# Kernel optimization log

Measured on AMD Instinct MI355X. Metric: run time of the kernel, lower is better.

## Reference

```python
import jax, jax.numpy as jnp
import numpy as np

N_NODES = 100000
N_EDGES = 1600000
N_GRAPHS = 2048
DIM_IN, DIM_H, DIM_FC, DIM_OUT = 128, 128, 256, 8


def _glorot(key, shape):
    fan_in, fan_out = shape[0], shape[1]
    lim = float(np.sqrt(6.0 / (fan_in + fan_out)))
    return jax.random.uniform(key, shape, jnp.float32, -lim, lim)


def setup_inputs() -> dict:
    key = jax.random.key(0)
    ks = jax.random.split(key, 16)
    x = jax.random.normal(ks[0], (N_NODES, DIM_IN), jnp.float32)
    edge_index = jax.random.randint(ks[1], (2, N_EDGES), 0, N_NODES, jnp.int64)
    batch = jnp.sort(jax.random.randint(ks[2], (N_NODES,), 0, N_GRAPHS, jnp.int64))
    inp = {"x": x, "edge_index": edge_index, "batch": batch}
    # GraphConv layers: W_rel [in,out], W_root [in,out], b [out]
    dims = [(DIM_IN, DIM_H), (DIM_H, DIM_H), (DIM_H, DIM_H), (DIM_H, DIM_H)]
    for i, (di, do) in enumerate(dims, start=1):
        inp[f"W{i}_rel"] = _glorot(ks[2 + 3 * i], (di, do))
        inp[f"W{i}_root"] = _glorot(ks[3 + 3 * i], (di, do))
        inp[f"b{i}"] = jnp.zeros((do,), jnp.float32)
    inp["fc_w"] = _glorot(ks[3], (DIM_H, DIM_FC))
    inp["fc_b"] = jnp.zeros((DIM_FC,), jnp.float32)
    inp["reg_w"] = _glorot(ks[4], (DIM_FC, DIM_OUT))
    inp["reg_b"] = jnp.zeros((DIM_OUT,), jnp.float32)
    return inp


def _graph_conv(x, src, dst, w_rel, w_root, b):
    # PyG GraphConv (aggr='add'): out_i = W_rel @ sum_{j->i} x_j + W_root @ x_i + b
    agg = jax.ops.segment_sum(x[src], dst, num_segments=N_NODES)  # [N, d_in]
    return agg @ w_rel + x @ w_root + b


def reference(x, edge_index, batch,
              W1_rel, W1_root, b1, W2_rel, W2_root, b2,
              W3_rel, W3_root, b3, W4_rel, W4_root, b4,
              fc_w, fc_b, reg_w, reg_b):
    src, dst = edge_index[0], edge_index[1]
    h = jax.nn.relu(_graph_conv(x, src, dst, W1_rel, W1_root, b1))
    h = jax.nn.relu(_graph_conv(h, src, dst, W2_rel, W2_root, b2))
    h = jax.nn.relu(_graph_conv(h, src, dst, W3_rel, W3_root, b3))
    h = jax.nn.relu(_graph_conv(h, src, dst, W4_rel, W4_root, b4))
    # global_mean_pool over graphs
    sums = jax.ops.segment_sum(h, batch, num_segments=N_GRAPHS)  # [G, d]
    cnt = jax.ops.segment_sum(jnp.ones((h.shape[0],), h.dtype), batch,
                              num_segments=N_GRAPHS)
    pooled = sums / jnp.maximum(cnt, 1.0)[:, None]
    # dropout is identity at inference
    hfc = pooled @ fc_w + fc_b
    return hfc @ reg_w + reg_b  # [G, dim_out]
```

## Files before the change

kernel.cpp:

```cpp
#include <hip/hip_runtime.h>

#define N_NODES 100000
#define N_EDGES 1600000
#define N_GRAPHS 2048
#define DIM 128

#define NBUK 196
#define BUKSH 9
#define NCH 256
#define EPB 6250
#define NMAT (NBUK * NCH)

typedef short short8v __attribute__((ext_vector_type(8)));
typedef float float4v __attribute__((ext_vector_type(4)));

__device__ __forceinline__ unsigned short f2bf(float f) {
  union { float f; unsigned u; } x; x.f = f;
  unsigned r = x.u + 0x7fffu + ((x.u >> 16) & 1u);
  return (unsigned short)(r >> 16);
}
__device__ __forceinline__ float bfhi2f(unsigned bits) {
  union { unsigned u; float f; } x; x.u = bits; return x.f;
}
__device__ __forceinline__ void accum8(float* p, uint4 v) {
  p[0] += bfhi2f(v.x << 16); p[1] += bfhi2f(v.x & 0xffff0000u);
  p[2] += bfhi2f(v.y << 16); p[3] += bfhi2f(v.y & 0xffff0000u);
  p[4] += bfhi2f(v.z << 16); p[5] += bfhi2f(v.z & 0xffff0000u);
  p[6] += bfhi2f(v.w << 16); p[7] += bfhi2f(v.w & 0xffff0000u);
}

__global__ __launch_bounds__(256) void k_bcount(const int* __restrict__ dst, int* __restrict__ cntmat) {
  __shared__ int cnt[NBUK];
  int b = blockIdx.x, t = threadIdx.x;
  if (t < NBUK) cnt[t] = 0;
  __syncthreads();
  int e0 = b * EPB;
  for (int j = t; j < EPB; j += 256) atomicAdd(&cnt[dst[e0 + j] >> BUKSH], 1);
  __syncthreads();
  if (t < NBUK) cntmat[t * NCH + b] = cnt[t];
}

__global__ __launch_bounds__(256) void k_scan1g(const int* __restrict__ in, int n,
                                                int* __restrict__ tmp, int* __restrict__ bsum) {
  __shared__ int sh[256];
  int b = blockIdx.x, t = threadIdx.x;
  int base = b * 1024 + t * 4;
  int v[4], s = 0;
#pragma unroll
  for (int i = 0; i < 4; i++) { v[i] = (base + i < n) ? in[base + i] : 0; s += v[i]; }
  sh[t] = s;
  __syncthreads();
  for (int off = 1; off < 256; off <<= 1) {
    int x = (t >= off) ? sh[t - off] : 0;
    __syncthreads();
    sh[t] += x;
    __syncthreads();
  }
  int run = sh[t] - s;
#pragma unroll
  for (int i = 0; i < 4; i++) { run += v[i]; if (base + i < n) tmp[base + i] = run; }
  if (t == 255) bsum[b] = sh[255];
}

__global__ void k_scan2g(int* __restrict__ bsum, int nb) {
  __shared__ int sh[128];
  int t = threadIdx.x;
  int v = (t < nb) ? bsum[t] : 0;
  sh[t] = v;
  __syncthreads();
  for (int off = 1; off < 128; off <<= 1) {
    int x = (t >= off) ? sh[t - off] : 0;
    __syncthreads();
    sh[t] += x;
    __syncthreads();
  }
  if (t < nb) bsum[t] = sh[t] - v;
}

__global__ __launch_bounds__(256) void k_exc(const int* __restrict__ tmp, const int* __restrict__ bsum,
                                             const int* __restrict__ in, int n, int* __restrict__ outExc) {
  int i = blockIdx.x * 256 + threadIdx.x;
  if (i < n) outExc[i] = tmp[i] + bsum[i >> 10] - in[i];
}

__global__ __launch_bounds__(256) void k_bscatter(const int* __restrict__ src, const int* __restrict__ dst,
                                                  const int* __restrict__ base, int2* __restrict__ epk) {
  __shared__ int cur[NBUK];
  int b = blockIdx.x, t = threadIdx.x;
  if (t < NBUK) cur[t] = base[t * NCH + b];
  __syncthreads();
  int e0 = b * EPB;
  for (int j = t; j < EPB; j += 256) {
    int s = src[e0 + j], d = dst[e0 + j];
    int pos = atomicAdd(&cur[d >> BUKSH], 1);
    epk[pos] = make_int2(s, d);
  }
}

__global__ __launch_bounds__(256) void k_bfinish(const int2* __restrict__ epk, const int* __restrict__ base,
                                                 int* __restrict__ rowptr, int* __restrict__ col) {
  __shared__ int a[512];
  __shared__ int sh[256];
  int k = blockIdx.x, t = threadIdx.x;
  int bstart = base[k * NCH];
  int bend = (k + 1 < NBUK) ? base[(k + 1) * NCH] : N_EDGES;
  a[t] = 0; a[t + 256] = 0;
  __syncthreads();
  for (int i = bstart + t; i < bend; i += 256) atomicAdd(&a[epk[i].y - (k << BUKSH)], 1);
  __syncthreads();
  int c0 = a[2 * t], c1 = a[2 * t + 1];
  int s = c0 + c1;
  sh[t] = s;
  __syncthreads();
  for (int off = 1; off < 256; off <<= 1) {
    int x = (t >= off) ? sh[t - off] : 0;
    __syncthreads();
    sh[t] += x;
    __syncthreads();
  }
  int excl = sh[t] - s;
  int st0 = bstart + excl;
  int st1 = st0 + c0;
  int g0 = (k << BUKSH) + 2 * t, g1 = g0 + 1;
  if (g0 < N_NODES) rowptr[g0] = st0;
  if (g1 < N_NODES) rowptr[g1] = st1;
  if (k == NBUK - 1 && t == 0) rowptr[N_NODES] = N_EDGES;
  __syncthreads();
  a[2 * t] = st0; a[2 * t + 1] = st1;
  __syncthreads();
  for (int i = bstart + t; i < bend; i += 256) {
    int2 e = epk[i];
    int pos = atomicAdd(&a[e.y - (k << BUKSH)], 1);
    col[pos] = e.x;
  }
}

__global__ __launch_bounds__(256) void k_gptr(const int* __restrict__ batch, int* __restrict__ gptr) {
  int i = blockIdx.x * 256 + threadIdx.x;
  if (i >= N_NODES) return;
  int b = batch[i];
  int a = (i == 0) ? -1 : batch[i - 1];
  for (int g = a + 1; g <= b; g++) gptr[g] = i;
  if (i == N_NODES - 1) {
    for (int g = b + 1; g <= N_GRAPHS; g++) gptr[g] = N_NODES;
  }
}

__global__ __launch_bounds__(256) void k_cvtx(const float* __restrict__ x, unsigned short* __restrict__ h) {
  int i = blockIdx.x * 256 + threadIdx.x;
  if (i < N_NODES * DIM / 4) {
    float4 v = ((const float4*)x)[i];
    unsigned lo = (unsigned)f2bf(v.x) | ((unsigned)f2bf(v.y) << 16);
    unsigned hi = (unsigned)f2bf(v.z) | ((unsigned)f2bf(v.w) << 16);
    ((uint2*)h)[i] = make_uint2(lo, hi);
  }
}

__global__ __launch_bounds__(256) void k_cvtw(const float* w0, const float* w1, const float* w2, const float* w3,
                                              const float* w4, const float* w5, const float* w6, const float* w7,
                                              unsigned short* __restrict__ wbF) {
  int i = blockIdx.x * 256 + threadIdx.x;
  if (i < 4 * 8 * 8 * 64 * 8) {
    int j = i & 7, l = (i >> 3) & 63, c = (i >> 9) & 7, kc = (i >> 12) & 7, layer = i >> 15;
    int m = layer * 2 + (kc >> 2);
    const float* w;
    switch (m) {
      case 0: w = w0; break; case 1: w = w1; break; case 2: w = w2; break; case 3: w = w3; break;
      case 4: w = w4; break; case 5: w = w5; break; case 6: w = w6; break; default: w = w7; break;
    }
    int kin = (kc & 3) * 32 + ((l >> 4) * 8) + j;
    int n = c * 16 + (l & 15);
    wbF[i] = f2bf(w[kin * 128 + n]);
  }
}

__global__ __launch_bounds__(256) void k_agg(const int* __restrict__ rowptr, const int* __restrict__ col,
                                             const unsigned short* __restrict__ hIn,
                                             unsigned short* __restrict__ aggOut) {
  int node = blockIdx.x * 4 + (threadIdx.x >> 6);
  if (node >= N_NODES) return;
  int lane = threadIdx.x & 63;
  int sub = lane >> 4;
  int li = lane & 15;
  int s0 = rowptr[node], s1 = rowptr[node + 1];
  float p[8];
#pragma unroll
  for (int j = 0; j < 8; j++) p[j] = 0.f;

  int e = s0;
  for (; e + 16 <= s1; e += 16) {
    int c0 = col[e + sub];
    int c1 = col[e + 4 + sub];
    int c2 = col[e + 8 + sub];
    int c3 = col[e + 12 + sub];
    uint4 v0 = *(const uint4*)(hIn + (size_t)c0 * DIM + li * 8);
    uint4 v1 = *(const uint4*)(hIn + (size_t)c1 * DIM + li * 8);
    uint4 v2 = *(const uint4*)(hIn + (size_t)c2 * DIM + li * 8);
    uint4 v3 = *(const uint4*)(hIn + (size_t)c3 * DIM + li * 8);
    accum8(p, v0);
    accum8(p, v1);
    accum8(p, v2);
    accum8(p, v3);
  }
  if (e + 8 <= s1) {
    int c0 = col[e + sub];
    int c1 = col[e + 4 + sub];
    uint4 v0 = *(const uint4*)(hIn + (size_t)c0 * DIM + li * 8);
    uint4 v1 = *(const uint4*)(hIn + (size_t)c1 * DIM + li * 8);
    accum8(p, v0);
    accum8(p, v1);
    e += 8;
  }
  if (e + 4 <= s1) {
    int c0 = col[e + sub];
    uint4 v0 = *(const uint4*)(hIn + (size_t)c0 * DIM + li * 8);
    accum8(p, v0);
    e += 4;
  }
  if (e + sub < s1) {
    int c0 = col[e + sub];
    uint4 v0 = *(const uint4*)(hIn + (size_t)c0 * DIM + li * 8);
    accum8(p, v0);
  }

#pragma unroll
  for (int j = 0; j < 8; j++) {
    p[j] += __shfl_xor(p[j], 16, 64);
    p[j] += __shfl_xor(p[j], 32, 64);
  }

  if (sub == 0) {
    uint4 o;
    o.x = (unsigned)f2bf(p[0]) | ((unsigned)f2bf(p[1]) << 16);
    o.y = (unsigned)f2bf(p[2]) | ((unsigned)f2bf(p[3]) << 16);
    o.z = (unsigned)f2bf(p[4]) | ((unsigned)f2bf(p[5]) << 16);
    o.w = (unsigned)f2bf(p[6]) | ((unsigned)f2bf(p[7]) << 16);
    *(uint4*)(aggOut + (size_t)node * DIM + li * 8) = o;
  }
}

__global__ __launch_bounds__(256, 4) void k_conv(const unsigned short* __restrict__ aggB,
                                                 const unsigned short* __restrict__ hIn,
                                                 const unsigned short* __restrict__ wbF,
                                                 const float* __restrict__ bias,
                                                 unsigned short* __restrict__ hOut) {
  __shared__ uint4 As[2048];
  const int t = threadIdx.x;
  const int row0b = blockIdx.x * 128;
  const int wave = t >> 6, lane = t & 63;

  float4v acc[2][8];
#pragma unroll
  for (int r = 0; r < 2; r++)
#pragma unroll
    for (int c = 0; c < 8; c++)
#pragma unroll
      for (int i = 0; i < 4; i++) acc[r][c][i] = 0.f;

#pragma unroll
  for (int phase = 0; phase < 2; phase++) {
    const unsigned short* Asrc = phase ? hIn : aggB;
#pragma unroll
    for (int j = 0; j < 8; j++) {
      int r = j * 16 + (t >> 4);
      int c = t & 15;
      int rsrc = row0b + r; if (rsrc > N_NODES - 1) rsrc = N_NODES - 1;
      uint4 v = *(const uint4*)(Asrc + (size_t)rsrc * DIM + c * 8);
      As[((r >> 4) * 16 + c) * 16 + ((r & 15) ^ c)] = v;
    }
    __syncthreads();

#pragma unroll
    for (int kc = 0; kc < 4; kc++) {
      short8v afr[2];
#pragma unroll
      for (int r = 0; r < 2; r++) {
        int g = wave * 2 + r;
        int c = kc * 4 + (lane >> 4);
        int rr = (lane & 15) ^ c;
        afr[r] = *(const short8v*)&As[(g * 16 + c) * 16 + rr];
      }
      int kcw = phase * 4 + kc;
#pragma unroll
      for (int c = 0; c < 8; c++) {
        short8v bfr = *(const short8v*)(wbF + (size_t)((kcw * 8 + c) * 64 + lane) * 8);
#pragma unroll
        for (int r = 0; r < 2; r++)
          acc[r][c] = __builtin_amdgcn_mfma_f32_16x16x32_bf16(afr[r], bfr, acc[r][c], 0, 0, 0);
      }
    }
    __syncthreads();
  }

  const int row0 = row0b + wave * 32;
#pragma unroll
  for (int r = 0; r < 2; r++) {
    int rbase = row0 + r * 16 + (lane >> 4) * 4;
#pragma unroll
    for (int c = 0; c < 8; c++) {
      int colidx = c * 16 + (lane & 15);
      float bv = bias[colidx];
#pragma unroll
      for (int i = 0; i < 4; i++) {
        int row = rbase + i;
        if (row < N_NODES) {
          float v = acc[r][c][i] + bv;
          v = v > 0.f ? v : 0.f;
          hOut[row * DIM + colidx] = f2bf(v);
        }
      }
    }
  }
}

__global__ __launch_bounds__(256) void k_pool(const unsigned short* __restrict__ h,
                                              const int* __restrict__ gptr,
                                              float* __restrict__ pooledMean) {
  int g = blockIdx.x * 4 + (threadIdx.x >> 6);
  if (g >= N_GRAPHS) return;
  int lane = threadIdx.x & 63;
  int li = lane & 15;
  int s0 = gptr[g], s1 = gptr[g + 1];
  float p[8];
#pragma unroll
  for (int j = 0; j < 8; j++) p[j] = 0.f;
  int f1 = s1 * 16;
  for (int f = s0 * 16 + lane; f < f1; f += 64) {
    uint4 v = ((const uint4*)h)[f];
    accum8(p, v);
  }
#pragma unroll
  for (int j = 0; j < 8; j++) {
    p[j] += __shfl_xor(p[j], 16, 64);
    p[j] += __shfl_xor(p[j], 32, 64);
  }
  float inv = (s1 > s0) ? 1.f / (float)(s1 - s0) : 0.f;
  if (lane < 16) {
    float4 o0 = make_float4(p[0] * inv, p[1] * inv, p[2] * inv, p[3] * inv);
    float4 o1 = make_float4(p[4] * inv, p[5] * inv, p[6] * inv, p[7] * inv);
    *(float4*)(pooledMean + g * DIM + li * 8) = o0;
    *(float4*)(pooledMean + g * DIM + li * 8 + 4) = o1;
  }
}

__global__ __launch_bounds__(256) void k_fc(const float* __restrict__ pooledMean,
                                            const float* __restrict__ fc_w, const float* __restrict__ fc_b,
                                            const float* __restrict__ reg_w, const float* __restrict__ reg_b,
                                            float* __restrict__ out) {
  __shared__ float sp[128];
  __shared__ float shfc[256];
  __shared__ float red[64];
  int g = blockIdx.x, t = threadIdx.x;
  if (t < 128) sp[t] = pooledMean[g * DIM + t];
  __syncthreads();
  float a = fc_b[t];
  for (int k = 0; k < 128; k++) a += sp[k] * fc_w[k * 256 + t];
  shfc[t] = a;
  __syncthreads();
  if (t < 64) {
    int o = t & 7, seg = t >> 3;
    float r = 0.f;
    for (int j = seg * 32; j < seg * 32 + 32; j++) r += shfc[j] * reg_w[j * 8 + o];
    red[t] = r;
  }
  __syncthreads();
  if (t < 8) {
    float r = reg_b[t];
    for (int s = 0; s < 8; s++) r += red[s * 8 + t];
    out[g * 8 + t] = r;
  }
}

extern "C" void kernel_launch(void* const* d_in, const int* in_sizes, int n_in,
                              void* d_out, int out_size, void* d_ws, size_t ws_size,
                              hipStream_t stream) {
  (void)in_sizes; (void)n_in; (void)out_size; (void)ws_size;
  const float* x = (const float*)d_in[0];
  const int* ei = (const int*)d_in[1];
  const int* src = ei;
  const int* dst = ei + N_EDGES;
  const int* batch = (const int*)d_in[2];
  const float* Wrel[4]  = {(const float*)d_in[3], (const float*)d_in[6], (const float*)d_in[9],  (const float*)d_in[12]};
  const float* Wroot[4] = {(const float*)d_in[4], (const float*)d_in[7], (const float*)d_in[10], (const float*)d_in[13]};
  const float* bias[4]  = {(const float*)d_in[5], (const float*)d_in[8], (const float*)d_in[11], (const float*)d_in[14]};
  const float* fc_w  = (const float*)d_in[15];
  const float* fc_b  = (const float*)d_in[16];
  const float* reg_w = (const float*)d_in[17];
  const float* reg_b = (const float*)d_in[18];
  float* out = (float*)d_out;

  char* ws = (char*)d_ws;
  size_t off = 0;
  auto alloc = [&](size_t b) -> char* {
    char* p = ws + off;
    off = (off + b + 255) & ~(size_t)255;
    return p;
  };
  int* rowptr = (int*)alloc((N_NODES + 1) * 4);
  int* cntmat = (int*)alloc((size_t)NMAT * 4);
  int* tmpB   = (int*)alloc((size_t)NMAT * 4);
  int* bsumB  = (int*)alloc(128 * 4);
  int* base   = (int*)alloc((size_t)NMAT * 4);
  int2* epk   = (int2*)alloc((size_t)N_EDGES * 8);
  int* colws  = (int*)alloc((size_t)N_EDGES * 4);
  int* gptr   = (int*)alloc((N_GRAPHS + 1) * 4);
  unsigned short* wbF = (unsigned short*)alloc((size_t)4 * 32768 * 2);
  unsigned short* h_a = (unsigned short*)alloc((size_t)N_NODES * DIM * 2);
  unsigned short* h_b = (unsigned short*)alloc((size_t)N_NODES * DIM * 2);
  unsigned short* agg = (unsigned short*)alloc((size_t)N_NODES * DIM * 2);
  float* pooled = (float*)alloc((size_t)N_GRAPHS * DIM * 4);

  k_bcount<<<NCH, 256, 0, stream>>>(dst, cntmat);
  k_scan1g<<<NMAT / 1024, 256, 0, stream>>>(cntmat, NMAT, tmpB, bsumB);
  k_scan2g<<<1, 128, 0, stream>>>(bsumB, NMAT / 1024);
  k_exc<<<(NMAT + 255) / 256, 256, 0, stream>>>(tmpB, bsumB, cntmat, NMAT, base);
  k_bscatter<<<NCH, 256, 0, stream>>>(src, dst, base, epk);
  k_bfinish<<<NBUK, 256, 0, stream>>>(epk, base, rowptr, colws);

  k_gptr<<<(N_NODES + 255) / 256, 256, 0, stream>>>(batch, gptr);
  k_cvtx<<<(N_NODES * DIM / 4 + 255) / 256, 256, 0, stream>>>(x, h_a);
  k_cvtw<<<(4 * 32768 + 255) / 256, 256, 0, stream>>>(
      Wrel[0], Wroot[0], Wrel[1], Wroot[1], Wrel[2], Wroot[2], Wrel[3], Wroot[3], wbF);

  unsigned short* h_in = h_a;
  unsigned short* h_out = h_b;
  for (int l = 0; l < 4; l++) {
    k_agg<<<(N_NODES + 3) / 4, 256, 0, stream>>>(rowptr, colws, h_in, agg);
    k_conv<<<(N_NODES + 127) / 128, 256, 0, stream>>>(
        agg, h_in, wbF + (size_t)l * 32768, bias[l], h_out);
    unsigned short* t2 = h_in; h_in = h_out; h_out = t2;
  }

  k_pool<<<(N_GRAPHS + 3) / 4, 256, 0, stream>>>(h_in, gptr, pooled);
  k_fc<<<N_GRAPHS, 256, 0, stream>>>(pooled, fc_w, fc_b, reg_w, reg_b, out);
}
```

Baseline: 521.5 us.

## Fuse neighbor aggregation into the GraphConv MFMA kernel via shared memory

Replaces the separate gather-aggregate kernel and the conv GEMM kernel with one fused kernel. Each wave aggregates neighbor features for its 16 nodes and writes the bf16 sums straight into the swizzled LDS tile, which then feeds the MFMA rel-weight phase. The root-weight phase reuses the same LDS buffer afterwards. This removes the global write and re-read of the aggregation buffer for every layer. In exchange there are far fewer concurrent waves issuing gathers, each wave processes its nodes one after another, and each weight fragment is reused over only 16 rows instead of 32, so gather latency hiding may get worse.

```diff
diff --git a/kernel.cpp b/kernel.cpp
--- a/kernel.cpp
+++ b/kernel.cpp
@@ -174,140 +174,128 @@
   }
 }
 
-__global__ __launch_bounds__(256) void k_agg(const int* __restrict__ rowptr, const int* __restrict__ col,
-                                             const unsigned short* __restrict__ hIn,
-                                             unsigned short* __restrict__ aggOut) {
-  int node = blockIdx.x * 4 + (threadIdx.x >> 6);
-  if (node >= N_NODES) return;
-  int lane = threadIdx.x & 63;
-  int sub = lane >> 4;
-  int li = lane & 15;
-  int s0 = rowptr[node], s1 = rowptr[node + 1];
-  float p[8];
-#pragma unroll
-  for (int j = 0; j < 8; j++) p[j] = 0.f;
-
-  int e = s0;
-  for (; e + 16 <= s1; e += 16) {
-    int c0 = col[e + sub];
-    int c1 = col[e + 4 + sub];
-    int c2 = col[e + 8 + sub];
-    int c3 = col[e + 12 + sub];
-    uint4 v0 = *(const uint4*)(hIn + (size_t)c0 * DIM + li * 8);
-    uint4 v1 = *(const uint4*)(hIn + (size_t)c1 * DIM + li * 8);
-    uint4 v2 = *(const uint4*)(hIn + (size_t)c2 * DIM + li * 8);
-    uint4 v3 = *(const uint4*)(hIn + (size_t)c3 * DIM + li * 8);
-    accum8(p, v0);
-    accum8(p, v1);
-    accum8(p, v2);
-    accum8(p, v3);
-  }
-  if (e + 8 <= s1) {
-    int c0 = col[e + sub];
-    int c1 = col[e + 4 + sub];
-    uint4 v0 = *(const uint4*)(hIn + (size_t)c0 * DIM + li * 8);
-    uint4 v1 = *(const uint4*)(hIn + (size_t)c1 * DIM + li * 8);
-    accum8(p, v0);
-    accum8(p, v1);
-    e += 8;
-  }
-  if (e + 4 <= s1) {
-    int c0 = col[e + sub];
-    uint4 v0 = *(const uint4*)(hIn + (size_t)c0 * DIM + li * 8);
-    accum8(p, v0);
-    e += 4;
-  }
-  if (e + sub < s1) {
-    int c0 = col[e + sub];
-    uint4 v0 = *(const uint4*)(hIn + (size_t)c0 * DIM + li * 8);
-    accum8(p, v0);
-  }
-
-#pragma unroll
-  for (int j = 0; j < 8; j++) {
-    p[j] += __shfl_xor(p[j], 16, 64);
-    p[j] += __shfl_xor(p[j], 32, 64);
-  }
-
-  if (sub == 0) {
-    uint4 o;
-    o.x = (unsigned)f2bf(p[0]) | ((unsigned)f2bf(p[1]) << 16);
-    o.y = (unsigned)f2bf(p[2]) | ((unsigned)f2bf(p[3]) << 16);
-    o.z = (unsigned)f2bf(p[4]) | ((unsigned)f2bf(p[5]) << 16);
-    o.w = (unsigned)f2bf(p[6]) | ((unsigned)f2bf(p[7]) << 16);
-    *(uint4*)(aggOut + (size_t)node * DIM + li * 8) = o;
-  }
-}
-
-__global__ __launch_bounds__(256, 4) void k_conv(const unsigned short* __restrict__ aggB,
-                                                 const unsigned short* __restrict__ hIn,
-                                                 const unsigned short* __restrict__ wbF,
-                                                 const float* __restrict__ bias,
-                                                 unsigned short* __restrict__ hOut) {
+__global__ __launch_bounds__(512, 4) void k_fused(const int* __restrict__ rowptr,
+                                                  const int* __restrict__ col,
+                                                  const unsigned short* __restrict__ hIn,
+                                                  const unsigned short* __restrict__ wbF,
+                                                  const float* __restrict__ bias,
+                                                  unsigned short* __restrict__ hOut) {
   __shared__ uint4 As[2048];
   const int t = threadIdx.x;
-  const int row0b = blockIdx.x * 128;
   const int wave = t >> 6, lane = t & 63;
-
-  float4v acc[2][8];
-#pragma unroll
-  for (int r = 0; r < 2; r++)
-#pragma unroll
-    for (int c = 0; c < 8; c++)
-#pragma unroll
-      for (int i = 0; i < 4; i++) acc[r][c][i] = 0.f;
-
-#pragma unroll
-  for (int phase = 0; phase < 2; phase++) {
-    const unsigned short* Asrc = phase ? hIn : aggB;
+  const int wrow0 = blockIdx.x * 128 + wave * 16;
+  const int sub = lane >> 4, li = lane & 15;
+
+  for (int ri = 0; ri < 16; ri++) {
+    int node = wrow0 + ri;
+    float p[8];
+#pragma unroll
+    for (int j = 0; j < 8; j++) p[j] = 0.f;
+    if (node < N_NODES) {
+      int s0 = rowptr[node], s1 = rowptr[node + 1];
+      int e = s0;
+      for (; e + 16 <= s1; e += 16) {
+        int c0 = col[e + sub];
+        int c1 = col[e + 4 + sub];
+        int c2 = col[e + 8 + sub];
+        int c3 = col[e + 12 + sub];
+        uint4 v0 = *(const uint4*)(hIn + (size_t)c0 * DIM + li * 8);
+        uint4 v1 = *(const uint4*)(hIn + (size_t)c1 * DIM + li * 8);
+        uint4 v2 = *(const uint4*)(hIn + (size_t)c2 * DIM + li * 8);
+        uint4 v3 = *(const uint4*)(hIn + (size_t)c3 * DIM + li * 8);
+        accum8(p, v0);
+        accum8(p, v1);
+        accum8(p, v2);
+        accum8(p, v3);
+      }
+      if (e + 8 <= s1) {
+        int c0 = col[e + sub];
+        int c1 = col[e + 4 + sub];
+        uint4 v0 = *(const uint4*)(hIn + (size_t)c0 * DIM + li * 8);
+        uint4 v1 = *(const uint4*)(hIn + (size_t)c1 * DIM + li * 8);
+        accum8(p, v0);
+        accum8(p, v1);
+        e += 8;
+      }
+      if (e + 4 <= s1) {
+        int c0 = col[e + sub];
+        uint4 v0 = *(const uint4*)(hIn + (size_t)c0 * DIM + li * 8);
+        accum8(p, v0);
+        e += 4;
+      }
+      if (e + sub < s1) {
+        int c0 = col[e + sub];
+        uint4 v0 = *(const uint4*)(hIn + (size_t)c0 * DIM + li * 8);
+        accum8(p, v0);
+      }
+    }
 #pragma unroll
     for (int j = 0; j < 8; j++) {
-      int r = j * 16 + (t >> 4);
-      int c = t & 15;
-      int rsrc = row0b + r; if (rsrc > N_NODES - 1) rsrc = N_NODES - 1;
-      uint4 v = *(const uint4*)(Asrc + (size_t)rsrc * DIM + c * 8);
-      As[((r >> 4) * 16 + c) * 16 + ((r & 15) ^ c)] = v;
-    }
-    __syncthreads();
-
-#pragma unroll
-    for (int kc = 0; kc < 4; kc++) {
-      short8v afr[2];
-#pragma unroll
-      for (int r = 0; r < 2; r++) {
-        int g = wave * 2 + r;
-        int c = kc * 4 + (lane >> 4);
-        int rr = (lane & 15) ^ c;
-        afr[r] = *(const short8v*)&As[(g * 16 + c) * 16 + rr];
-      }
-      int kcw = phase * 4 + kc;
-#pragma unroll
-      for (int c = 0; c < 8; c++) {
-        short8v bfr = *(const short8v*)(wbF + (size_t)((kcw * 8 + c) * 64 + lane) * 8);
-#pragma unroll
-        for (int r = 0; r < 2; r++)
-          acc[r][c] = __builtin_amdgcn_mfma_f32_16x16x32_bf16(afr[r], bfr, acc[r][c], 0, 0, 0);
-      }
-    }
-    __syncthreads();
-  }
-
-  const int row0 = row0b + wave * 32;
-#pragma unroll
-  for (int r = 0; r < 2; r++) {
-    int rbase = row0 + r * 16 + (lane >> 4) * 4;
-#pragma unroll
-    for (int c = 0; c < 8; c++) {
-      int colidx = c * 16 + (lane & 15);
-      float bv = bias[colidx];
-#pragma unroll
-      for (int i = 0; i < 4; i++) {
-        int row = rbase + i;
-        if (row < N_NODES) {
-          float v = acc[r][c][i] + bv;
-          v = v > 0.f ? v : 0.f;
-          hOut[row * DIM + colidx] = f2bf(v);
-        }
+      p[j] += __shfl_xor(p[j], 16, 64);
+      p[j] += __shfl_xor(p[j], 32, 64);
+    }
+    if (sub == 0) {
+      uint4 o;
+      o.x = (unsigned)f2bf(p[0]) | ((unsigned)f2bf(p[1]) << 16);
+      o.y = (unsigned)f2bf(p[2]) | ((unsigned)f2bf(p[3]) << 16);
+      o.z = (unsigned)f2bf(p[4]) | ((unsigned)f2bf(p[5]) << 16);
+      o.w = (unsigned)f2bf(p[6]) | ((unsigned)f2bf(p[7]) << 16);
+      As[(wave * 16 + li) * 16 + (ri ^ li)] = o;
+    }
+  }
+  __syncthreads();
+
+  float4v acc[8];
+#pragma unroll
+  for (int c2 = 0; c2 < 8; c2++)
+#pragma unroll
+    for (int i = 0; i < 4; i++) acc[c2][i] = 0.f;
+
+#pragma unroll
+  for (int kc = 0; kc < 4; kc++) {
+    int c = kc * 4 + sub;
+    short8v afr = *(const short8v*)&As[(wave * 16 + c) * 16 + (li ^ c)];
+#pragma unroll
+    for (int c2 = 0; c2 < 8; c2++) {
+      short8v bfr = *(const short8v*)(wbF + (size_t)((kc * 8 + c2) * 64 + lane) * 8);
+      acc[c2] = __builtin_amdgcn_mfma_f32_16x16x32_bf16(afr, bfr, acc[c2], 0, 0, 0);
+    }
+  }
+  __syncthreads();
+
+#pragma unroll
+  for (int j = 0; j < 4; j++) {
+    int idx = j * 64 + lane;
+    int r = idx >> 4, c = idx & 15;
+    int rsrc = wrow0 + r; if (rsrc > N_NODES - 1) rsrc = N_NODES - 1;
+    uint4 v = *(const uint4*)(hIn + (size_t)rsrc * DIM + c * 8);
+    As[(wave * 16 + c) * 16 + (r ^ c)] = v;
+  }
+  __syncthreads();
+
+#pragma unroll
+  for (int kc = 0; kc < 4; kc++) {
+    int c = kc * 4 + sub;
+    short8v afr = *(const short8v*)&As[(wave * 16 + c) * 16 + (li ^ c)];
+#pragma unroll
+    for (int c2 = 0; c2 < 8; c2++) {
+      short8v bfr = *(const short8v*)(wbF + (size_t)(((4 + kc) * 8 + c2) * 64 + lane) * 8);
+      acc[c2] = __builtin_amdgcn_mfma_f32_16x16x32_bf16(afr, bfr, acc[c2], 0, 0, 0);
+    }
+  }
+
+  int rbase = wrow0 + sub * 4;
+#pragma unroll
+  for (int c2 = 0; c2 < 8; c2++) {
+    int colidx = c2 * 16 + li;
+    float bv = bias[colidx];
+#pragma unroll
+    for (int i = 0; i < 4; i++) {
+      int row = rbase + i;
+      if (row < N_NODES) {
+        float v = acc[c2][i] + bv;
+        v = v > 0.f ? v : 0.f;
+        hOut[row * DIM + colidx] = f2bf(v);
       }
     }
   }
@@ -407,7 +395,6 @@
   unsigned short* wbF = (unsigned short*)alloc((size_t)4 * 32768 * 2);
   unsigned short* h_a = (unsigned short*)alloc((size_t)N_NODES * DIM * 2);
   unsigned short* h_b = (unsigned short*)alloc((size_t)N_NODES * DIM * 2);
-  unsigned short* agg = (unsigned short*)alloc((size_t)N_NODES * DIM * 2);
   float* pooled = (float*)alloc((size_t)N_GRAPHS * DIM * 4);
 
   k_bcount<<<NCH, 256, 0, stream>>>(dst, cntmat);
@@ -424,10 +411,9 @@
 
   unsigned short* h_in = h_a;
   unsigned short* h_out = h_b;
+  const int FB = (N_NODES + 127) / 128;
   for (int l = 0; l < 4; l++) {
-    k_agg<<<(N_NODES + 3) / 4, 256, 0, stream>>>(rowptr, colws, h_in, agg);
-    k_conv<<<(N_NODES + 127) / 128, 256, 0, stream>>>(
-        agg, h_in, wbF + (size_t)l * 32768, bias[l], h_out);
+    k_fused<<<FB, 512, 0, stream>>>(rowptr, colws, h_in, wbF + (size_t)l * 32768, bias[l], h_out);
     unsigned short* t2 = h_in; h_in = h_out; h_out = t2;
   }
 
```

New measurement: 622.5 us. 19.4% more time.
